# Kernel optimization log

Measured on AMD Instinct MI355X. Metric: run time of the kernel, lower is better.

Reference implementation:

```python
import jax, jax.numpy as jnp
import numpy as np

SPIXELS = 1000
CLASSES = 21


def setup_inputs() -> dict:
    key = jax.random.key(0)
    k1, k2, k3, k4 = jax.random.split(key, 4)
    B, H, W = 8, 512, 512
    pred = jax.random.normal(k1, (B, CLASSES, H, W), dtype=jnp.float32)
    Laplace_W_c = jax.random.normal(k2, (B, SPIXELS, SPIXELS), dtype=jnp.float32)
    Laplace_L_c = jax.random.normal(k3, (B, SPIXELS, SPIXELS), dtype=jnp.float32)
    image_spiex = jax.random.randint(k4, (B, H, W), 0, SPIXELS, dtype=jnp.int32)
    return {"pred": pred, "Laplace_W_c": Laplace_W_c, "Laplace_L_c": Laplace_L_c, "image_spiex": image_spiex}


def reference(pred, Laplace_W_c, Laplace_L_c, image_spiex):
    B, _, H, W = pred.shape
    P = H * W
    # Faithful to original: permute(0,2,3,1) then reshape to [B, class_num, H*W]
    pred_r = jnp.transpose(pred, (0, 2, 3, 1)).reshape(B, CLASSES, P)  # [B, C, P]
    seg = image_spiex.reshape(B, P)  # [B, P] superpixel ids
    # result[b, c, s] = sum_{p: seg[b,p]==s} pred_r[b, c, p]  -- the bmm(pred, one_hot_mask)
    # expressed as an efficient segment-sum instead of materializing [B, P, SPIXELS].
    seg_sum = jax.vmap(
        lambda x, ids: jax.ops.segment_sum(x, ids, num_segments=SPIXELS)
    )(jnp.transpose(pred_r, (0, 2, 1)), seg)  # [B, S, C]
    result = jnp.transpose(seg_sum, (0, 2, 1))  # [B, C, S]
    # mask.sum() = count of (b, p, s) with seg[b,p] == s, i.e. pixels with valid ids
    mask_sum = jnp.sum(((seg >= 0) & (seg < SPIXELS)).astype(pred.dtype))
    result = result / (mask_sum + 1e-16)
    # trace(R @ L @ R^T) per batch, fused
    traces = jnp.einsum('bcs,bst,bct->b', result, Laplace_L_c, result)  # [B]
    loss = (2.0 / jnp.linalg.norm(Laplace_W_c)) * traces
    return jnp.mean(loss)
```

## Files before the change

### kernel.cpp

```cpp
#include <hip/hip_runtime.h>
#include <hip/hip_bf16.h>

#define SPIX 1000
#define NCLS 21
#define PP (512*512)
#define NB_IMG 8
#define EPB (NCLS*PP)

#define FWIN 32768
#define BLKS_PER_B (EPB / FWIN)
#define DUMP 1000

#define R_OFF   0
#define TR_OFF  (NB_IMG*NCLS*SPIX)
#define NS_OFF  (TR_OFF + NB_IMG)
#define CNT_OFF (NS_OFF + 1)
#define CTR_OFF (CNT_OFF + 1)
#define WS_FLOATS (CTR_OFF + 1)

__device__ __forceinline__ void fatomic_add(float* p, float v) {
    unsafeAtomicAdd(p, v);
}

#define CLOBBER() asm volatile("" ::: "memory")

__global__ __launch_bounds__(512, 8) void scatter_kernel(const float* __restrict__ pred,
                                                         const int* __restrict__ seg,
                                                         const float* __restrict__ W,
                                                         float* __restrict__ Rout,
                                                         float* __restrict__ ns,
                                                         float* __restrict__ cnt) {
    if (blockIdx.y == NB_IMG) {
        if (blockIdx.x < 128) {
            const float4* W4 = (const float4*)W;
            const int n4 = (NB_IMG * SPIX * SPIX) / 4;
            float s = 0.f;
            for (int i = blockIdx.x * 512 + threadIdx.x; i < n4; i += 128 * 512) {
                float4 v = W4[i];
                s += v.x*v.x + v.y*v.y + v.z*v.z + v.w*v.w;
            }
            #pragma unroll
            for (int off = 32; off; off >>= 1) s += __shfl_xor(s, off);
            if ((threadIdx.x & 63) == 0) fatomic_add(ns, s);
        } else {
            const int4* s4 = (const int4*)seg;
            const int n4 = (NB_IMG * PP) / 4;
            int c = 0;
            for (int i = (blockIdx.x - 128) * 512 + threadIdx.x; i < n4; i += 40 * 512) {
                int4 v = s4[i];
                c += ((unsigned)v.x < SPIX) + ((unsigned)v.y < SPIX) + ((unsigned)v.z < SPIX) + ((unsigned)v.w < SPIX);
            }
            float f = (float)c;
            #pragma unroll
            for (int off = 32; off; off >>= 1) f += __shfl_xor(f, off);
            if ((threadIdx.x & 63) == 0) fatomic_add(cnt, f);
        }
        return;
    }
    __shared__ float          Rw[8][1024];
    __shared__ unsigned short Mk[8][1024];
    const int b    = blockIdx.y;
    const int tid  = threadIdx.x;
    const int wave = tid >> 6;
    const unsigned short lane = (unsigned short)(tid & 63);
    const unsigned f0 = (unsigned)blockIdx.x * FWIN;
    const unsigned c0 = f0 >> 18;
    const unsigned p0 = f0 & (PP - 1);

    for (int i = tid; i < 8 * 1024; i += 512) ((float*)Rw)[i] = 0.f;
    __syncthreads();

    float*          wR = Rw[wave];
    unsigned short* wM = Mk[wave];

    const float* pb   = pred + (size_t)b * EPB;
    const int*   segb = seg + (size_t)b * PP + p0;

#define PREF(E0, SV, VV) do {                                     \
        SV = *(const int4*)(segb + (E0));                         \
        unsigned fk = f0 + (unsigned)(E0);                        \
        unsigned sp = fk / 21u;                                   \
        unsigned ch = fk - sp * 21u;                              \
        _Pragma("unroll")                                         \
        for (int k = 0; k < 4; ++k) {                             \
            VV[k] = pb[(ch << 18) + sp];                          \
            ch++;                                                 \
            bool c21 = (ch == 21u);                               \
            sp += c21 ? 1u : 0u;                                  \
            ch  = c21 ? 0u : ch;                                  \
        }                                                         \
    } while (0)

    int4 svN; float vN[4];
    PREF(tid * 4, svN, vN);

    for (int it = 0; it < FWIN / (512 * 4); ++it) {
        int4 sv = svN;
        float vA[4] = {vN[0], vN[1], vN[2], vN[3]};
        if (it + 1 < FWIN / (512 * 4)) {
            PREF(((it + 1) * 512 + tid) * 4, svN, vN);
        }
        int sA[4];
        #pragma unroll
        for (int k = 0; k < 4; ++k) {
            int s = (&sv.x)[k];
            sA[k] = ((unsigned)s < SPIX) ? s : DUMP;
        }
        #pragma unroll
        for (int i = 0; i < 3; ++i)
            #pragma unroll
            for (int j = i + 1; j < 4; ++j) {
                bool e = (sA[j] == sA[i]) && (sA[i] != DUMP);
                vA[i] += e ? vA[j] : 0.f;
                sA[j]  = e ? DUMP  : sA[j];
            }
        #pragma unroll
        for (int k = 0; k < 4; ++k) wM[sA[k]] = lane;
        CLOBBER();
        unsigned short rd[4];
        #pragma unroll
        for (int k = 0; k < 4; ++k) rd[k] = wM[sA[k]];
        CLOBBER();
        float od[4];
        #pragma unroll
        for (int k = 0; k < 4; ++k) od[k] = wR[sA[k]];
        CLOBBER();
        bool lose1[4];
        #pragma unroll
        for (int k = 0; k < 4; ++k) {
            lose1[k] = (rd[k] != lane);
            wR[lose1[k] ? DUMP : sA[k]] = od[k] + vA[k];
        }
        CLOBBER();
        #pragma unroll
        for (int k = 0; k < 4; ++k) {
            if (lose1[k]) fatomic_add(&wR[sA[k]], vA[k]);
        }
    }
#undef PREF
    __syncthreads();

    float* Rb = Rout + (size_t)b * NCLS * SPIX + (size_t)c0 * SPIX;
    for (int i = tid; i < SPIX; i += 512) {
        float a = 0.f;
        #pragma unroll
        for (int w = 0; w < 8; ++w) a += Rw[w][i];
        fatomic_add(&Rb[i], a);
    }
}

__global__ __launch_bounds__(512) void trace_kernel(const float* __restrict__ L,
                                                    const float* __restrict__ R,
                                                    float* __restrict__ traces,
                                                    const float* __restrict__ ns,
                                                    const float* __restrict__ cnt,
                                                    unsigned* __restrict__ ctr,
                                                    float* __restrict__ out) {
    __shared__ float Rl[NCLS * SPIX];
    const int b = blockIdx.y;
    const float* Rb = R + (size_t)b * NCLS * SPIX;
    for (int i = threadIdx.x; i < NCLS * SPIX; i += 512) Rl[i] = Rb[i];
    __syncthreads();

    const int wave = threadIdx.x >> 6;
    const int lane = threadIdx.x & 63;
    const float* Lb = L + (size_t)b * SPIX * SPIX;

    const int s0 = (blockIdx.x * 8 + wave) * 4;
    bool val[4];
    const float4* Lr[4];
    #pragma unroll
    for (int r = 0; r < 4; ++r) {
        int sr = s0 + r;
        val[r] = sr < SPIX;
        Lr[r] = (const float4*)(Lb + (size_t)(val[r] ? sr : (SPIX - 1)) * SPIX);
    }

    float acc[4][NCLS];
    #pragma unroll
    for (int r = 0; r < 4; ++r)
        #pragma unroll
        for (int c = 0; c < NCLS; ++c) acc[r][c] = 0.f;

    #pragma unroll
    for (int it = 0; it < 4; ++it) {
        int idx = it * 64 + lane;
        if (idx < SPIX / 4) {
            float4 l[4];
            #pragma unroll
            for (int r = 0; r < 4; ++r)
                l[r] = val[r] ? Lr[r][idx] : make_float4(0.f, 0.f, 0.f, 0.f);
            #pragma unroll
            for (int c = 0; c < NCLS; ++c) {
                float4 rr = *(const float4*)&Rl[c * SPIX + idx * 4];
                #pragma unroll
                for (int r = 0; r < 4; ++r)
                    acc[r][c] += l[r].x * rr.x + l[r].y * rr.y + l[r].z * rr.z + l[r].w * rr.w;
            }
        }
    }

    float partial = 0.f;
    #pragma unroll
    for (int c = 0; c < NCLS; ++c)
        #pragma unroll
        for (int r = 0; r < 4; ++r)
            if (val[r]) partial += Rl[c * SPIX + s0 + r] * acc[r][c];

    #pragma unroll
    for (int off = 32; off; off >>= 1) partial += __shfl_xor(partial, off);
    if (lane == 0) fatomic_add(&traces[b], partial);

    __syncthreads();
    if (threadIdx.x == 0) {
        __threadfence();
        unsigned old = atomicAdd(ctr, 1u);
        if (old == 32u * NB_IMG - 1u) {
            __threadfence();
            float t = 0.f;
            #pragma unroll
            for (int i = 0; i < NB_IMG; ++i)
                t += __hip_atomic_load(&traces[i], __ATOMIC_RELAXED, __HIP_MEMORY_SCOPE_AGENT);
            float denom = cnt[0] + 1e-16f;
            out[0] = (2.f / sqrtf(ns[0])) * t / (denom * denom) / (float)NB_IMG;
        }
    }
}

extern "C" void kernel_launch(void* const* d_in, const int* in_sizes, int n_in,
                              void* d_out, int out_size, void* d_ws, size_t ws_size,
                              hipStream_t stream) {
    const float* pred = (const float*)d_in[0];
    const float* Wc   = (const float*)d_in[1];
    const float* Lc   = (const float*)d_in[2];
    const int*   seg  = (const int*)d_in[3];
    float* ws = (float*)d_ws;
    float* out = (float*)d_out;

    hipMemsetAsync(d_ws, 0, WS_FLOATS * sizeof(float), stream);

    scatter_kernel<<<dim3(BLKS_PER_B, NB_IMG + 1), 512, 0, stream>>>(
        pred, seg, Wc, ws + R_OFF, ws + NS_OFF, ws + CNT_OFF);

    trace_kernel<<<dim3(32, NB_IMG), 512, 0, stream>>>(
        Lc, ws + R_OFF, ws + TR_OFF, ws + NS_OFF, ws + CNT_OFF,
        (unsigned*)(ws + CTR_OFF), out);
}
```

Measured before the change: 141.6 us.

## Process two classes per scatter block to share segment lookups

Restructures the segment-sum scatter so each block handles a pixel window for two output classes, reusing one segment-id load and one conflict-resolution pass for both. This halves the per-class seg loads and LDS owner-mark traffic, at the cost of double-size LDS accumulators, lower occupancy (launch bound 4), and an odd last class group. It also skips zero-valued global atomics in the final flush and rebalances the auxiliary norm and count blocks.

```diff
diff --git a/kernel.cpp b/kernel.cpp
--- a/kernel.cpp
+++ b/kernel.cpp
@@ -7,9 +7,12 @@
 #define NB_IMG 8
 #define EPB (NCLS*PP)
 
-#define FWIN 32768
-#define BLKS_PER_B (EPB / FWIN)
+#define PPIX 16384
+#define PWPB (PP/PPIX)
+#define NCG 11
+#define GX (PWPB*NCG)
 #define DUMP 1000
+#define SP21 12483
 
 #define R_OFF   0
 #define TR_OFF  (NB_IMG*NCLS*SPIX)
@@ -24,18 +27,18 @@
 
 #define CLOBBER() asm volatile("" ::: "memory")
 
-__global__ __launch_bounds__(512, 8) void scatter_kernel(const float* __restrict__ pred,
+__global__ __launch_bounds__(512, 4) void scatter_kernel(const float* __restrict__ pred,
                                                          const int* __restrict__ seg,
                                                          const float* __restrict__ W,
                                                          float* __restrict__ Rout,
                                                          float* __restrict__ ns,
                                                          float* __restrict__ cnt) {
     if (blockIdx.y == NB_IMG) {
-        if (blockIdx.x < 128) {
+        if (blockIdx.x < 88) {
             const float4* W4 = (const float4*)W;
             const int n4 = (NB_IMG * SPIX * SPIX) / 4;
             float s = 0.f;
-            for (int i = blockIdx.x * 512 + threadIdx.x; i < n4; i += 128 * 512) {
+            for (int i = blockIdx.x * 512 + threadIdx.x; i < n4; i += 88 * 512) {
                 float4 v = W4[i];
                 s += v.x*v.x + v.y*v.y + v.z*v.z + v.w*v.w;
             }
@@ -46,7 +49,7 @@
             const int4* s4 = (const int4*)seg;
             const int n4 = (NB_IMG * PP) / 4;
             int c = 0;
-            for (int i = (blockIdx.x - 128) * 512 + threadIdx.x; i < n4; i += 40 * 512) {
+            for (int i = (blockIdx.x - 88) * 512 + threadIdx.x; i < n4; i += 88 * 512) {
                 int4 v = s4[i];
                 c += ((unsigned)v.x < SPIX) + ((unsigned)v.y < SPIX) + ((unsigned)v.z < SPIX) + ((unsigned)v.w < SPIX);
             }
@@ -57,17 +60,19 @@
         }
         return;
     }
-    __shared__ float          Rw[8][1024];
+    __shared__ float          Rw[8][2048];
     __shared__ unsigned short Mk[8][1024];
-    const int b    = blockIdx.y;
+    const int b   = blockIdx.y;
+    const int pw  = blockIdx.x & (PWPB - 1);
+    const int cg  = blockIdx.x >> 4;
+    const int c0  = cg * 2;
+    const bool two = (cg < 10);
     const int tid  = threadIdx.x;
     const int wave = tid >> 6;
     const unsigned short lane = (unsigned short)(tid & 63);
-    const unsigned f0 = (unsigned)blockIdx.x * FWIN;
-    const unsigned c0 = f0 >> 18;
-    const unsigned p0 = f0 & (PP - 1);
-
-    for (int i = tid; i < 8 * 1024; i += 512) ((float*)Rw)[i] = 0.f;
+    const unsigned p0 = (unsigned)pw * PPIX;
+
+    for (int i = tid; i < 8 * 2048; i += 512) ((float*)Rw)[i] = 0.f;
     __syncthreads();
 
     float*          wR = Rw[wave];
@@ -76,29 +81,36 @@
     const float* pb   = pred + (size_t)b * EPB;
     const int*   segb = seg + (size_t)b * PP + p0;
 
-#define PREF(E0, SV, VV) do {                                     \
-        SV = *(const int4*)(segb + (E0));                         \
-        unsigned fk = f0 + (unsigned)(E0);                        \
-        unsigned sp = fk / 21u;                                   \
-        unsigned ch = fk - sp * 21u;                              \
-        _Pragma("unroll")                                         \
-        for (int k = 0; k < 4; ++k) {                             \
-            VV[k] = pb[(ch << 18) + sp];                          \
-            ch++;                                                 \
-            bool c21 = (ch == 21u);                               \
-            sp += c21 ? 1u : 0u;                                  \
-            ch  = c21 ? 0u : ch;                                  \
-        }                                                         \
+#define PREF(E0, SV, VA, VB) do {                                  \
+        SV = *(const int4*)(segb + (E0));                          \
+        unsigned f  = (unsigned)c0 * PP + p0 + (unsigned)(E0);     \
+        unsigned sp = f / 21u;                                     \
+        unsigned ch = f - sp * 21u;                                \
+        _Pragma("unroll")                                          \
+        for (int k = 0; k < 4; ++k) {                              \
+            VA[k] = pb[(ch << 18) + sp];                           \
+            if (two) {                                             \
+                unsigned c1 = ch + 1u, s1 = sp + SP21;             \
+                bool cr = (c1 == 21u);                             \
+                c1 = cr ? 0u : c1; s1 += cr ? 1u : 0u;             \
+                VB[k] = pb[(c1 << 18) + s1];                       \
+            }                                                      \
+            ch++;                                                  \
+            bool cc = (ch == 21u);                                 \
+            sp += cc ? 1u : 0u;                                    \
+            ch  = cc ? 0u : ch;                                    \
+        }                                                          \
     } while (0)
 
-    int4 svN; float vN[4];
-    PREF(tid * 4, svN, vN);
-
-    for (int it = 0; it < FWIN / (512 * 4); ++it) {
+    int4 svN; float vNA[4], vNB[4];
+    PREF(tid * 4, svN, vNA, vNB);
+
+    for (int it = 0; it < PPIX / (512 * 4); ++it) {
         int4 sv = svN;
-        float vA[4] = {vN[0], vN[1], vN[2], vN[3]};
-        if (it + 1 < FWIN / (512 * 4)) {
-            PREF(((it + 1) * 512 + tid) * 4, svN, vN);
+        float vA[4] = {vNA[0], vNA[1], vNA[2], vNA[3]};
+        float vB[4] = {vNB[0], vNB[1], vNB[2], vNB[3]};
+        if (it + 1 < PPIX / (512 * 4)) {
+            PREF(((it + 1) * 512 + tid) * 4, svN, vNA, vNB);
         }
         int sA[4];
         #pragma unroll
@@ -112,6 +124,7 @@
             for (int j = i + 1; j < 4; ++j) {
                 bool e = (sA[j] == sA[i]) && (sA[i] != DUMP);
                 vA[i] += e ? vA[j] : 0.f;
+                vB[i] += e ? vB[j] : 0.f;
                 sA[j]  = e ? DUMP  : sA[j];
             }
         #pragma unroll
@@ -121,31 +134,45 @@
         #pragma unroll
         for (int k = 0; k < 4; ++k) rd[k] = wM[sA[k]];
         CLOBBER();
-        float od[4];
-        #pragma unroll
-        for (int k = 0; k < 4; ++k) od[k] = wR[sA[k]];
+        float od0[4], od1[4];
+        #pragma unroll
+        for (int k = 0; k < 4; ++k) od0[k] = wR[sA[k] * 2];
+        if (two) {
+            #pragma unroll
+            for (int k = 0; k < 4; ++k) od1[k] = wR[sA[k] * 2 + 1];
+        }
         CLOBBER();
         bool lose1[4];
         #pragma unroll
         for (int k = 0; k < 4; ++k) {
             lose1[k] = (rd[k] != lane);
-            wR[lose1[k] ? DUMP : sA[k]] = od[k] + vA[k];
+            wR[lose1[k] ? 2000 : (sA[k] * 2)] = od0[k] + vA[k];
+        }
+        if (two) {
+            #pragma unroll
+            for (int k = 0; k < 4; ++k)
+                wR[lose1[k] ? 2001 : (sA[k] * 2 + 1)] = od1[k] + vB[k];
         }
         CLOBBER();
         #pragma unroll
         for (int k = 0; k < 4; ++k) {
-            if (lose1[k]) fatomic_add(&wR[sA[k]], vA[k]);
+            if (lose1[k]) {
+                fatomic_add(&wR[sA[k] * 2], vA[k]);
+                if (two) fatomic_add(&wR[sA[k] * 2 + 1], vB[k]);
+            }
         }
     }
 #undef PREF
     __syncthreads();
 
     float* Rb = Rout + (size_t)b * NCLS * SPIX + (size_t)c0 * SPIX;
-    for (int i = tid; i < SPIX; i += 512) {
+    for (int i = tid; i < 2000; i += 512) {
+        int cls = i & 1, s = i >> 1;
+        if (cls && !two) continue;
         float a = 0.f;
         #pragma unroll
         for (int w = 0; w < 8; ++w) a += Rw[w][i];
-        fatomic_add(&Rb[i], a);
+        if (a != 0.f) fatomic_add(&Rb[cls * SPIX + s], a);
     }
 }
 
@@ -239,7 +266,7 @@
 
     hipMemsetAsync(d_ws, 0, WS_FLOATS * sizeof(float), stream);
 
-    scatter_kernel<<<dim3(BLKS_PER_B, NB_IMG + 1), 512, 0, stream>>>(
+    scatter_kernel<<<dim3(GX, NB_IMG + 1), 512, 0, stream>>>(
         pred, seg, Wc, ws + R_OFF, ws + NS_OFF, ws + CNT_OFF);
 
     trace_kernel<<<dim3(32, NB_IMG), 512, 0, stream>>>(
```

Measured after the change: 150.9 us. 6.5% more time.

## Fuse scatter and trace kernels into one launch with per-batch spin-wait flags

Applied to the files above, without the earlier changes.

Merges the scatter, scalar-reduction and trace kernels into a single launch. Per-batch done counters let trace blocks for a batch start as soon as that batch's scatter finishes, so the trace work on L overlaps with scatter work on other batches and the second launch and its tail disappear. Trace blocks now read R directly from global memory instead of staging it in LDS, and handle 2 rows per wave across 63 blocks per batch. The spin-waits rely on the producer blocks being scheduled before or alongside the waiters; block index ordering makes that likely but not guaranteed, and launch bounds drop to 4 blocks per SM.

```diff
diff --git a/kernel.cpp b/kernel.cpp
--- a/kernel.cpp
+++ b/kernel.cpp
@@ -11,12 +11,20 @@
 #define BLKS_PER_B (EPB / FWIN)
 #define DUMP 1000
 
+#define NSCAT (BLKS_PER_B * NB_IMG)
+#define NSCAL 168
+#define TXB 63
+#define NTRC (TXB * NB_IMG)
+#define NBLKS (NSCAT + NSCAL + NTRC)
+
 #define R_OFF   0
 #define TR_OFF  (NB_IMG*NCLS*SPIX)
 #define NS_OFF  (TR_OFF + NB_IMG)
 #define CNT_OFF (NS_OFF + 1)
-#define CTR_OFF (CNT_OFF + 1)
-#define WS_FLOATS (CTR_OFF + 1)
+#define DONE_OFF (CNT_OFF + 1)
+#define SD_OFF  (DONE_OFF + NB_IMG)
+#define CT_OFF  (SD_OFF + 1)
+#define WS_FLOATS (CT_OFF + 1)
 
 __device__ __forceinline__ void fatomic_add(float* p, float v) {
     unsafeAtomicAdd(p, v);
@@ -24,57 +32,43 @@
 
 #define CLOBBER() asm volatile("" ::: "memory")
 
-__global__ __launch_bounds__(512, 8) void scatter_kernel(const float* __restrict__ pred,
-                                                         const int* __restrict__ seg,
-                                                         const float* __restrict__ W,
-                                                         float* __restrict__ Rout,
-                                                         float* __restrict__ ns,
-                                                         float* __restrict__ cnt) {
-    if (blockIdx.y == NB_IMG) {
-        if (blockIdx.x < 128) {
-            const float4* W4 = (const float4*)W;
-            const int n4 = (NB_IMG * SPIX * SPIX) / 4;
-            float s = 0.f;
-            for (int i = blockIdx.x * 512 + threadIdx.x; i < n4; i += 128 * 512) {
-                float4 v = W4[i];
-                s += v.x*v.x + v.y*v.y + v.z*v.z + v.w*v.w;
-            }
-            #pragma unroll
-            for (int off = 32; off; off >>= 1) s += __shfl_xor(s, off);
-            if ((threadIdx.x & 63) == 0) fatomic_add(ns, s);
-        } else {
-            const int4* s4 = (const int4*)seg;
-            const int n4 = (NB_IMG * PP) / 4;
-            int c = 0;
-            for (int i = (blockIdx.x - 128) * 512 + threadIdx.x; i < n4; i += 40 * 512) {
-                int4 v = s4[i];
-                c += ((unsigned)v.x < SPIX) + ((unsigned)v.y < SPIX) + ((unsigned)v.z < SPIX) + ((unsigned)v.w < SPIX);
-            }
-            float f = (float)c;
-            #pragma unroll
-            for (int off = 32; off; off >>= 1) f += __shfl_xor(f, off);
-            if ((threadIdx.x & 63) == 0) fatomic_add(cnt, f);
-        }
-        return;
-    }
+__global__ __launch_bounds__(512, 4) void fused_kernel(const float* __restrict__ pred,
+                                                       const int* __restrict__ seg,
+                                                       const float* __restrict__ W,
+                                                       const float* __restrict__ L,
+                                                       float* __restrict__ ws,
+                                                       float* __restrict__ out) {
     __shared__ float          Rw[8][1024];
     __shared__ unsigned short Mk[8][1024];
-    const int b    = blockIdx.y;
-    const int tid  = threadIdx.x;
-    const int wave = tid >> 6;
-    const unsigned short lane = (unsigned short)(tid & 63);
-    const unsigned f0 = (unsigned)blockIdx.x * FWIN;
-    const unsigned c0 = f0 >> 18;
-    const unsigned p0 = f0 & (PP - 1);
-
-    for (int i = tid; i < 8 * 1024; i += 512) ((float*)Rw)[i] = 0.f;
-    __syncthreads();
-
-    float*          wR = Rw[wave];
-    unsigned short* wM = Mk[wave];
-
-    const float* pb   = pred + (size_t)b * EPB;
-    const int*   segb = seg + (size_t)b * PP + p0;
+
+    float* Rbase   = ws + R_OFF;
+    float* traces  = ws + TR_OFF;
+    float* ns      = ws + NS_OFF;
+    float* cnt     = ws + CNT_OFF;
+    unsigned* done = (unsigned*)(ws + DONE_OFF);
+    unsigned* sd   = (unsigned*)(ws + SD_OFF);
+    unsigned* ct   = (unsigned*)(ws + CT_OFF);
+
+    const int blk = blockIdx.x;
+    const int tid = threadIdx.x;
+
+    if (blk < NSCAT) {
+        const int b   = blk / BLKS_PER_B;
+        const int sub = blk % BLKS_PER_B;
+        const int wave = tid >> 6;
+        const unsigned short lane = (unsigned short)(tid & 63);
+        const unsigned f0 = (unsigned)sub * FWIN;
+        const unsigned c0 = f0 >> 18;
+        const unsigned p0 = f0 & (PP - 1);
+
+        for (int i = tid; i < 8 * 1024; i += 512) ((float*)Rw)[i] = 0.f;
+        __syncthreads();
+
+        float*          wR = Rw[wave];
+        unsigned short* wM = Mk[wave];
+
+        const float* pb   = pred + (size_t)b * EPB;
+        const int*   segb = seg + (size_t)b * PP + p0;
 
 #define PREF(E0, SV, VV) do {                                     \
         SV = *(const int4*)(segb + (E0));                         \
@@ -91,138 +85,165 @@
         }                                                         \
     } while (0)
 
-    int4 svN; float vN[4];
-    PREF(tid * 4, svN, vN);
-
-    for (int it = 0; it < FWIN / (512 * 4); ++it) {
-        int4 sv = svN;
-        float vA[4] = {vN[0], vN[1], vN[2], vN[3]};
-        if (it + 1 < FWIN / (512 * 4)) {
-            PREF(((it + 1) * 512 + tid) * 4, svN, vN);
-        }
-        int sA[4];
-        #pragma unroll
-        for (int k = 0; k < 4; ++k) {
-            int s = (&sv.x)[k];
-            sA[k] = ((unsigned)s < SPIX) ? s : DUMP;
-        }
-        #pragma unroll
-        for (int i = 0; i < 3; ++i)
-            #pragma unroll
-            for (int j = i + 1; j < 4; ++j) {
-                bool e = (sA[j] == sA[i]) && (sA[i] != DUMP);
-                vA[i] += e ? vA[j] : 0.f;
-                sA[j]  = e ? DUMP  : sA[j];
-            }
-        #pragma unroll
-        for (int k = 0; k < 4; ++k) wM[sA[k]] = lane;
-        CLOBBER();
-        unsigned short rd[4];
-        #pragma unroll
-        for (int k = 0; k < 4; ++k) rd[k] = wM[sA[k]];
-        CLOBBER();
-        float od[4];
-        #pragma unroll
-        for (int k = 0; k < 4; ++k) od[k] = wR[sA[k]];
-        CLOBBER();
-        bool lose1[4];
-        #pragma unroll
-        for (int k = 0; k < 4; ++k) {
-            lose1[k] = (rd[k] != lane);
-            wR[lose1[k] ? DUMP : sA[k]] = od[k] + vA[k];
-        }
-        CLOBBER();
-        #pragma unroll
-        for (int k = 0; k < 4; ++k) {
-            if (lose1[k]) fatomic_add(&wR[sA[k]], vA[k]);
-        }
-    }
+        int4 svN; float vN[4];
+        PREF(tid * 4, svN, vN);
+
+        for (int it = 0; it < FWIN / (512 * 4); ++it) {
+            int4 sv = svN;
+            float vA[4] = {vN[0], vN[1], vN[2], vN[3]};
+            if (it + 1 < FWIN / (512 * 4)) {
+                PREF(((it + 1) * 512 + tid) * 4, svN, vN);
+            }
+            int sA[4];
+            #pragma unroll
+            for (int k = 0; k < 4; ++k) {
+                int s = (&sv.x)[k];
+                sA[k] = ((unsigned)s < SPIX) ? s : DUMP;
+            }
+            #pragma unroll
+            for (int i = 0; i < 3; ++i)
+                #pragma unroll
+                for (int j = i + 1; j < 4; ++j) {
+                    bool e = (sA[j] == sA[i]) && (sA[i] != DUMP);
+                    vA[i] += e ? vA[j] : 0.f;
+                    sA[j]  = e ? DUMP  : sA[j];
+                }
+            #pragma unroll
+            for (int k = 0; k < 4; ++k) wM[sA[k]] = lane;
+            CLOBBER();
+            unsigned short rd[4];
+            #pragma unroll
+            for (int k = 0; k < 4; ++k) rd[k] = wM[sA[k]];
+            CLOBBER();
+            float od[4];
+            #pragma unroll
+            for (int k = 0; k < 4; ++k) od[k] = wR[sA[k]];
+            CLOBBER();
+            bool lose1[4];
+            #pragma unroll
+            for (int k = 0; k < 4; ++k) {
+                lose1[k] = (rd[k] != lane);
+                wR[lose1[k] ? DUMP : sA[k]] = od[k] + vA[k];
+            }
+            CLOBBER();
+            #pragma unroll
+            for (int k = 0; k < 4; ++k) {
+                if (lose1[k]) fatomic_add(&wR[sA[k]], vA[k]);
+            }
+        }
 #undef PREF
-    __syncthreads();
-
-    float* Rb = Rout + (size_t)b * NCLS * SPIX + (size_t)c0 * SPIX;
-    for (int i = tid; i < SPIX; i += 512) {
-        float a = 0.f;
-        #pragma unroll
-        for (int w = 0; w < 8; ++w) a += Rw[w][i];
-        fatomic_add(&Rb[i], a);
-    }
-}
-
-__global__ __launch_bounds__(512) void trace_kernel(const float* __restrict__ L,
-                                                    const float* __restrict__ R,
-                                                    float* __restrict__ traces,
-                                                    const float* __restrict__ ns,
-                                                    const float* __restrict__ cnt,
-                                                    unsigned* __restrict__ ctr,
-                                                    float* __restrict__ out) {
-    __shared__ float Rl[NCLS * SPIX];
-    const int b = blockIdx.y;
-    const float* Rb = R + (size_t)b * NCLS * SPIX;
-    for (int i = threadIdx.x; i < NCLS * SPIX; i += 512) Rl[i] = Rb[i];
-    __syncthreads();
-
-    const int wave = threadIdx.x >> 6;
-    const int lane = threadIdx.x & 63;
-    const float* Lb = L + (size_t)b * SPIX * SPIX;
-
-    const int s0 = (blockIdx.x * 8 + wave) * 4;
-    bool val[4];
-    const float4* Lr[4];
-    #pragma unroll
-    for (int r = 0; r < 4; ++r) {
-        int sr = s0 + r;
-        val[r] = sr < SPIX;
-        Lr[r] = (const float4*)(Lb + (size_t)(val[r] ? sr : (SPIX - 1)) * SPIX);
-    }
-
-    float acc[4][NCLS];
-    #pragma unroll
-    for (int r = 0; r < 4; ++r)
-        #pragma unroll
-        for (int c = 0; c < NCLS; ++c) acc[r][c] = 0.f;
-
-    #pragma unroll
-    for (int it = 0; it < 4; ++it) {
-        int idx = it * 64 + lane;
-        if (idx < SPIX / 4) {
-            float4 l[4];
-            #pragma unroll
-            for (int r = 0; r < 4; ++r)
-                l[r] = val[r] ? Lr[r][idx] : make_float4(0.f, 0.f, 0.f, 0.f);
-            #pragma unroll
-            for (int c = 0; c < NCLS; ++c) {
-                float4 rr = *(const float4*)&Rl[c * SPIX + idx * 4];
+        __syncthreads();
+
+        float* Rbrow = Rbase + ((size_t)b * NCLS + c0) * SPIX;
+        for (int i = tid; i < SPIX; i += 512) {
+            float a = 0.f;
+            #pragma unroll
+            for (int w = 0; w < 8; ++w) a += Rw[w][i];
+            if (a != 0.f) fatomic_add(&Rbrow[i], a);
+        }
+        __syncthreads();
+        if (tid == 0)
+            __hip_atomic_fetch_add(&done[b], 1u, __ATOMIC_RELEASE, __HIP_MEMORY_SCOPE_AGENT);
+
+    } else if (blk < NSCAT + NSCAL) {
+        const int sb = blk - NSCAT;
+        if (sb < 128) {
+            const float4* W4 = (const float4*)W;
+            const int n4 = (NB_IMG * SPIX * SPIX) / 4;
+            float s = 0.f;
+            for (int i = sb * 512 + tid; i < n4; i += 128 * 512) {
+                float4 v = W4[i];
+                s += v.x*v.x + v.y*v.y + v.z*v.z + v.w*v.w;
+            }
+            #pragma unroll
+            for (int off = 32; off; off >>= 1) s += __shfl_xor(s, off);
+            if ((tid & 63) == 0) fatomic_add(ns, s);
+        } else {
+            const int4* s4 = (const int4*)seg;
+            const int n4 = (NB_IMG * PP) / 4;
+            int c = 0;
+            for (int i = (sb - 128) * 512 + tid; i < n4; i += 40 * 512) {
+                int4 v = s4[i];
+                c += ((unsigned)v.x < SPIX) + ((unsigned)v.y < SPIX) + ((unsigned)v.z < SPIX) + ((unsigned)v.w < SPIX);
+            }
+            float f = (float)c;
+            #pragma unroll
+            for (int off = 32; off; off >>= 1) f += __shfl_xor(f, off);
+            if ((tid & 63) == 0) fatomic_add(cnt, f);
+        }
+        __syncthreads();
+        if (tid == 0)
+            __hip_atomic_fetch_add(sd, 1u, __ATOMIC_RELEASE, __HIP_MEMORY_SCOPE_AGENT);
+
+    } else {
+        const int tb = blk - NSCAT - NSCAL;
+        const int b  = tb / TXB;
+        const int x  = tb % TXB;
+        const int wave = tid >> 6;
+        const int lane = tid & 63;
+
+        if (tid == 0) {
+            while (__hip_atomic_load(&done[b], __ATOMIC_ACQUIRE, __HIP_MEMORY_SCOPE_AGENT)
+                   < (unsigned)BLKS_PER_B)
+                __builtin_amdgcn_s_sleep(8);
+        }
+        __syncthreads();
+        __builtin_amdgcn_fence(__ATOMIC_ACQUIRE, "agent");
+
+        const float* Lb = L + (size_t)b * SPIX * SPIX;
+        const float* Rg = Rbase + (size_t)b * NCLS * SPIX;
+
+        const int s0 = (x * 8 + wave) * 2;
+        const int s1 = s0 + 1;
+        const bool v0 = s0 < SPIX, v1 = s1 < SPIX;
+        const float4* L40 = (const float4*)(Lb + (size_t)(v0 ? s0 : (SPIX - 1)) * SPIX);
+        const float4* L41 = (const float4*)(Lb + (size_t)(v1 ? s1 : (SPIX - 1)) * SPIX);
+
+        float acc0[NCLS], acc1[NCLS];
+        #pragma unroll
+        for (int c = 0; c < NCLS; ++c) { acc0[c] = 0.f; acc1[c] = 0.f; }
+
+        #pragma unroll
+        for (int it = 0; it < 4; ++it) {
+            int idx = it * 64 + lane;
+            if (idx < SPIX / 4) {
+                float4 l0 = v0 ? L40[idx] : make_float4(0.f, 0.f, 0.f, 0.f);
+                float4 l1 = v1 ? L41[idx] : make_float4(0.f, 0.f, 0.f, 0.f);
                 #pragma unroll
-                for (int r = 0; r < 4; ++r)
-                    acc[r][c] += l[r].x * rr.x + l[r].y * rr.y + l[r].z * rr.z + l[r].w * rr.w;
-            }
-        }
-    }
-
-    float partial = 0.f;
-    #pragma unroll
-    for (int c = 0; c < NCLS; ++c)
-        #pragma unroll
-        for (int r = 0; r < 4; ++r)
-            if (val[r]) partial += Rl[c * SPIX + s0 + r] * acc[r][c];
-
-    #pragma unroll
-    for (int off = 32; off; off >>= 1) partial += __shfl_xor(partial, off);
-    if (lane == 0) fatomic_add(&traces[b], partial);
-
-    __syncthreads();
-    if (threadIdx.x == 0) {
-        __threadfence();
-        unsigned old = atomicAdd(ctr, 1u);
-        if (old == 32u * NB_IMG - 1u) {
-            __threadfence();
-            float t = 0.f;
-            #pragma unroll
-            for (int i = 0; i < NB_IMG; ++i)
-                t += __hip_atomic_load(&traces[i], __ATOMIC_RELAXED, __HIP_MEMORY_SCOPE_AGENT);
-            float denom = cnt[0] + 1e-16f;
-            out[0] = (2.f / sqrtf(ns[0])) * t / (denom * denom) / (float)NB_IMG;
+                for (int c = 0; c < NCLS; ++c) {
+                    float4 rr = ((const float4*)(Rg + c * SPIX))[idx];
+                    acc0[c] += l0.x * rr.x + l0.y * rr.y + l0.z * rr.z + l0.w * rr.w;
+                    acc1[c] += l1.x * rr.x + l1.y * rr.y + l1.z * rr.z + l1.w * rr.w;
+                }
+            }
+        }
+
+        float partial = 0.f;
+        #pragma unroll
+        for (int c = 0; c < NCLS; ++c) {
+            if (v0) partial += Rg[c * SPIX + s0] * acc0[c];
+            if (v1) partial += Rg[c * SPIX + s1] * acc1[c];
+        }
+        #pragma unroll
+        for (int off = 32; off; off >>= 1) partial += __shfl_xor(partial, off);
+        if (lane == 0) fatomic_add(&traces[b], partial);
+
+        __syncthreads();
+        if (tid == 0) {
+            unsigned old = __hip_atomic_fetch_add(ct, 1u, __ATOMIC_ACQ_REL, __HIP_MEMORY_SCOPE_AGENT);
+            if (old == (unsigned)NTRC - 1u) {
+                while (__hip_atomic_load(sd, __ATOMIC_ACQUIRE, __HIP_MEMORY_SCOPE_AGENT)
+                       < (unsigned)NSCAL)
+                    __builtin_amdgcn_s_sleep(8);
+                float t = 0.f;
+                #pragma unroll
+                for (int i = 0; i < NB_IMG; ++i)
+                    t += __hip_atomic_load(&traces[i], __ATOMIC_RELAXED, __HIP_MEMORY_SCOPE_AGENT);
+                float nsv  = __hip_atomic_load(ns,  __ATOMIC_RELAXED, __HIP_MEMORY_SCOPE_AGENT);
+                float cntv = __hip_atomic_load(cnt, __ATOMIC_RELAXED, __HIP_MEMORY_SCOPE_AGENT);
+                float denom = cntv + 1e-16f;
+                out[0] = (2.f / sqrtf(nsv)) * t / (denom * denom) / (float)NB_IMG;
+            }
         }
     }
 }
@@ -237,12 +258,7 @@
     float* ws = (float*)d_ws;
     float* out = (float*)d_out;
 
-    hipMemsetAsync(d_ws, 0, WS_FLOATS * sizeof(float), stream);
-
-    scatter_kernel<<<dim3(BLKS_PER_B, NB_IMG + 1), 512, 0, stream>>>(
-        pred, seg, Wc, ws + R_OFF, ws + NS_OFF, ws + CNT_OFF);
-
-    trace_kernel<<<dim3(32, NB_IMG), 512, 0, stream>>>(
-        Lc, ws + R_OFF, ws + TR_OFF, ws + NS_OFF, ws + CNT_OFF,
-        (unsigned*)(ws + CTR_OFF), out);
+    (void)hipMemsetAsync(d_ws, 0, WS_FLOATS * sizeof(float), stream);
+
+    fused_kernel<<<NBLKS, 512, 0, stream>>>(pred, seg, Wc, Lc, ws, out);
 }
```

New measurement: 275.8 us. +94.8%, slower.

## Drop LDS staging in trace kernel and spread rows over more blocks

Applied to the files above, without the earlier changes.

The trace kernel no longer copies the 84KB R matrix into shared memory per block. It reads R directly from global memory (L2-cached) and processes two L rows per wave instead of four. The grid grows from 32 to 63 blocks per image, which removes the per-block staging cost and the LDS occupancy limit. The trade is more global/L2 traffic for R. The scatter kernel also skips atomic adds of zero partial sums.

```diff
diff --git a/kernel.cpp b/kernel.cpp
--- a/kernel.cpp
+++ b/kernel.cpp
@@ -10,6 +10,9 @@
 #define FWIN 32768
 #define BLKS_PER_B (EPB / FWIN)
 #define DUMP 1000
+
+#define TXB 63
+#define NTRC (TXB * NB_IMG)
 
 #define R_OFF   0
 #define TR_OFF  (NB_IMG*NCLS*SPIX)
@@ -145,7 +148,7 @@
         float a = 0.f;
         #pragma unroll
         for (int w = 0; w < 8; ++w) a += Rw[w][i];
-        fatomic_add(&Rb[i], a);
+        if (a != 0.f) fatomic_add(&Rb[i], a);
     }
 }
 
@@ -156,57 +159,43 @@
                                                     const float* __restrict__ cnt,
                                                     unsigned* __restrict__ ctr,
                                                     float* __restrict__ out) {
-    __shared__ float Rl[NCLS * SPIX];
     const int b = blockIdx.y;
-    const float* Rb = R + (size_t)b * NCLS * SPIX;
-    for (int i = threadIdx.x; i < NCLS * SPIX; i += 512) Rl[i] = Rb[i];
-    __syncthreads();
-
     const int wave = threadIdx.x >> 6;
     const int lane = threadIdx.x & 63;
     const float* Lb = L + (size_t)b * SPIX * SPIX;
-
-    const int s0 = (blockIdx.x * 8 + wave) * 4;
-    bool val[4];
-    const float4* Lr[4];
-    #pragma unroll
-    for (int r = 0; r < 4; ++r) {
-        int sr = s0 + r;
-        val[r] = sr < SPIX;
-        Lr[r] = (const float4*)(Lb + (size_t)(val[r] ? sr : (SPIX - 1)) * SPIX);
-    }
-
-    float acc[4][NCLS];
-    #pragma unroll
-    for (int r = 0; r < 4; ++r)
-        #pragma unroll
-        for (int c = 0; c < NCLS; ++c) acc[r][c] = 0.f;
+    const float* Rg = R + (size_t)b * NCLS * SPIX;
+
+    const int s0 = (blockIdx.x * 8 + wave) * 2;
+    const int s1 = s0 + 1;
+    const bool v0 = s0 < SPIX, v1 = s1 < SPIX;
+    const float4* L40 = (const float4*)(Lb + (size_t)(v0 ? s0 : (SPIX - 1)) * SPIX);
+    const float4* L41 = (const float4*)(Lb + (size_t)(v1 ? s1 : (SPIX - 1)) * SPIX);
+
+    float acc0[NCLS], acc1[NCLS];
+    #pragma unroll
+    for (int c = 0; c < NCLS; ++c) { acc0[c] = 0.f; acc1[c] = 0.f; }
 
     #pragma unroll
     for (int it = 0; it < 4; ++it) {
         int idx = it * 64 + lane;
         if (idx < SPIX / 4) {
-            float4 l[4];
-            #pragma unroll
-            for (int r = 0; r < 4; ++r)
-                l[r] = val[r] ? Lr[r][idx] : make_float4(0.f, 0.f, 0.f, 0.f);
+            float4 l0 = v0 ? L40[idx] : make_float4(0.f, 0.f, 0.f, 0.f);
+            float4 l1 = v1 ? L41[idx] : make_float4(0.f, 0.f, 0.f, 0.f);
             #pragma unroll
             for (int c = 0; c < NCLS; ++c) {
-                float4 rr = *(const float4*)&Rl[c * SPIX + idx * 4];
-                #pragma unroll
-                for (int r = 0; r < 4; ++r)
-                    acc[r][c] += l[r].x * rr.x + l[r].y * rr.y + l[r].z * rr.z + l[r].w * rr.w;
+                float4 rr = ((const float4*)(Rg + c * SPIX))[idx];
+                acc0[c] += l0.x * rr.x + l0.y * rr.y + l0.z * rr.z + l0.w * rr.w;
+                acc1[c] += l1.x * rr.x + l1.y * rr.y + l1.z * rr.z + l1.w * rr.w;
             }
         }
     }
 
     float partial = 0.f;
     #pragma unroll
-    for (int c = 0; c < NCLS; ++c)
-        #pragma unroll
-        for (int r = 0; r < 4; ++r)
-            if (val[r]) partial += Rl[c * SPIX + s0 + r] * acc[r][c];
-
+    for (int c = 0; c < NCLS; ++c) {
+        if (v0) partial += Rg[c * SPIX + s0] * acc0[c];
+        if (v1) partial += Rg[c * SPIX + s1] * acc1[c];
+    }
     #pragma unroll
     for (int off = 32; off; off >>= 1) partial += __shfl_xor(partial, off);
     if (lane == 0) fatomic_add(&traces[b], partial);
@@ -215,7 +204,7 @@
     if (threadIdx.x == 0) {
         __threadfence();
         unsigned old = atomicAdd(ctr, 1u);
-        if (old == 32u * NB_IMG - 1u) {
+        if (old == (unsigned)(TXB * NB_IMG) - 1u) {
             __threadfence();
             float t = 0.f;
             #pragma unroll
@@ -237,12 +226,12 @@
     float* ws = (float*)d_ws;
     float* out = (float*)d_out;
 
-    hipMemsetAsync(d_ws, 0, WS_FLOATS * sizeof(float), stream);
+    (void)hipMemsetAsync(d_ws, 0, WS_FLOATS * sizeof(float), stream);
 
     scatter_kernel<<<dim3(BLKS_PER_B, NB_IMG + 1), 512, 0, stream>>>(
         pred, seg, Wc, ws + R_OFF, ws + NS_OFF, ws + CNT_OFF);
 
-    trace_kernel<<<dim3(32, NB_IMG), 512, 0, stream>>>(
+    trace_kernel<<<dim3(TXB, NB_IMG), 512, 0, stream>>>(
         Lc, ws + R_OFF, ws + TR_OFF, ws + NS_OFF, ws + CNT_OFF,
         (unsigned*)(ws + CTR_OFF), out);
 }
```

Result: slower. 160.0 us (+13.0%).
